# Kernel tuning notes

Measured on AMD Instinct MI355X. Metric: run time of the kernel, lower is better.

## Reference

```python
import jax, jax.numpy as jnp
import numpy as np

NUM_ITER = 8  # num_iterations


def kernel_to_freq_2d(kernel, H, W):
    """Place a (C, kh, kw) kernel circularly centered at origin on an (H, W) grid, then FFT."""
    C, kh, kw = kernel.shape
    th = (jnp.arange(kh) - kh // 2) % H
    tw = (jnp.arange(kw) - kw // 2) % W
    TH, TW = jnp.meshgrid(th, tw, indexing='ij')
    padded = jnp.zeros((C, H, W), dtype=kernel.dtype).at[:, TH, TW].set(kernel)
    return jnp.fft.fft2(padded, axes=(1, 2))  # (C, H, W) complex


def setup_inputs() -> dict:
    key = jax.random.key(0)
    k1, k2, k3 = jax.random.split(key, 3)
    B, H, W, C, k = 8, 256, 256, 64, 7
    x = jax.random.normal(k1, (B, H, W, C), dtype=jnp.float32)
    # gate_kernel is zeros-init in the module; use small random values so the
    # gate path is non-degenerate while keeping identical math.
    gate_kernel = jax.random.normal(k2, (C, k, k), dtype=jnp.float32) * 0.02
    # hidden_kernel: lecun_normal over fan_in = k*k (param shape (C, k, k))
    hidden_kernel = jax.random.normal(k3, (C, k, k), dtype=jnp.float32) * (1.0 / np.sqrt(k * k))
    return {"x": x, "gate_kernel": gate_kernel, "hidden_kernel": hidden_kernel}


def reference(x, gate_kernel, hidden_kernel):
    B, H, W, C = x.shape
    # Frequency-domain depthwise kernels, laid out (H, W, C) to match channels-last state.
    gate_f = kernel_to_freq_2d(gate_kernel, H, W).transpose(1, 2, 0)
    hidden_f = kernel_to_freq_2d(hidden_kernel, H, W).transpose(1, 2, 0)

    def step(h, _):
        # FFT over spatial dims (equivalent to the original's transpose->fft->transpose).
        h_f = jnp.fft.fft2(h, axes=(1, 2))  # (B, H, W, C) complex
        z = jax.nn.sigmoid(jnp.fft.ifft2(gate_f[None] * h_f, axes=(1, 2)).real)
        h_tilde = jnp.fft.ifft2(hidden_f[None] * h_f, axes=(1, 2)).real
        h_new = (1 - z) * h + z * h_tilde
        return h_new, None

    h_final, _ = jax.lax.scan(step, x, None, length=NUM_ITER)
    return h_final.astype(x.dtype)
```

## Files before the change

### kernel.cpp

```cpp
#include <hip/hip_runtime.h>


#define HH 256
#define WW 256
#define CC 64
#define TH 8
#define BC 128
#define LHT (TH + 6)
#define LWT (BC + 6)
#define PLANE (LHT * LWT)
#define WOFF (4 * PLANE)
#define LDS_FLOATS (WOFF + 196)

__global__ __launch_bounds__(256, 4) void gated_step(
    const float* __restrict__ src,
    const float* __restrict__ wg_g,
    const float* __restrict__ wh_g,
    float* __restrict__ dst)
{
    __shared__ float lds[LDS_FLOATS];

    const int tid = threadIdx.x;
    const int x   = tid & 63;
    const int w   = __builtin_amdgcn_readfirstlane(tid >> 6);

    const int id  = (int)blockIdx.x;
    const int nid = ((id & 7) << 10) | (id >> 3);
    const int cg  = nid & 15;
    const int xs  = (nid >> 4) & 1;
    const int ys  = (nid >> 5) & 31;
    const int b   = nid >> 10;
    const int x0  = xs * BC;
    const int y0  = ys * TH;
    const int ch  = (cg << 2) | w;

    float sw[49];
    #pragma unroll
    for (int t = 0; t < 49; ++t)
        sw[t] = __int_as_float(
            __builtin_amdgcn_readfirstlane(__float_as_int(wg_g[ch * 49 + t])));

    const float4* __restrict__ src4 = reinterpret_cast<const float4*>(src);
    for (int k = tid; k < PLANE; k += 256) {
        int col = k % LWT;
        int row = k / LWT;
        int gy = (y0 + row - 3) & 255;
        int gx = (x0 + col - 3) & 255;
        float4 v4 = src4[((((b << 8) + gy) << 8) + gx) * 16 + cg];
        lds[0 * PLANE + k] = v4.x;
        lds[1 * PLANE + k] = v4.y;
        lds[2 * PLANE + k] = v4.z;
        lds[3 * PLANE + k] = v4.w;
    }
    if (tid < 196) lds[WOFF + tid] = wh_g[cg * 196 + tid];
    __syncthreads();

    float wh[49];
    #pragma unroll
    for (int t = 0; t < 49; ++t) wh[t] = lds[WOFF + w * 49 + t];

    const float* plane = &lds[w * PLANE];
    float accg[2][TH], acch[2][TH];
    #pragma unroll
    for (int r = 0; r < TH; ++r) {
        accg[0][r] = 0.0f; accg[1][r] = 0.0f;
        acch[0][r] = 0.0f; acch[1][r] = 0.0f;
    }

    #pragma unroll
    for (int iy = 0; iy < LHT; ++iy) {
        float v[8];
        const float* rowp = plane + iy * LWT + 2 * x;
        #pragma unroll
        for (int m = 0; m < 4; ++m) {
            float2 t2 = *reinterpret_cast<const float2*>(rowp + 2 * m);
            v[2 * m]     = t2.x;
            v[2 * m + 1] = t2.y;
        }
        #pragma unroll
        for (int r = 0; r < TH; ++r) {
            const int i = r + 6 - iy;
            if (i >= 0 && i <= 6) {
                #pragma unroll
                for (int jv = 0; jv < 7; ++jv) {
                    const float a = sw[i * 7 + (6 - jv)];
                    const float h = wh[i * 7 + (6 - jv)];
                    accg[0][r] = fmaf(a, v[jv],     accg[0][r]);
                    acch[0][r] = fmaf(h, v[jv],     acch[0][r]);
                    accg[1][r] = fmaf(a, v[jv + 1], accg[1][r]);
                    acch[1][r] = fmaf(h, v[jv + 1], acch[1][r]);
                }
            }
        }
    }

    float hn[2][TH];
    #pragma unroll
    for (int r = 0; r < TH; ++r) {
        float c0 = plane[(r + 3) * LWT + 2 * x + 3];
        float c1 = plane[(r + 3) * LWT + 2 * x + 4];
        float e0 = __expf(-accg[0][r]);
        float e1 = __expf(-accg[1][r]);
        float z0 = __builtin_amdgcn_rcpf(1.0f + e0);
        float z1 = __builtin_amdgcn_rcpf(1.0f + e1);
        hn[0][r] = fmaf(z0, acch[0][r] - c0, c0);
        hn[1][r] = fmaf(z1, acch[1][r] - c1, c1);
    }
    __syncthreads();

    #pragma unroll
    for (int r = 0; r < TH; ++r) {
        float2 p; p.x = hn[0][r]; p.y = hn[1][r];
        *reinterpret_cast<float2*>(&lds[w * 1024 + r * 128 + 2 * x]) = p;
    }
    __syncthreads();

    float4* __restrict__ dst4 = reinterpret_cast<float4*>(dst);
    #pragma unroll
    for (int k2 = 0; k2 < 4; ++k2) {
        int pos = tid + k2 * 256;
        int c2  = pos & 127;
        int r   = pos >> 7;
        float4 o;
        o.x = lds[0 * 1024 + r * 128 + c2];
        o.y = lds[1 * 1024 + r * 128 + c2];
        o.z = lds[2 * 1024 + r * 128 + c2];
        o.w = lds[3 * 1024 + r * 128 + c2];
        dst4[((((b << 8) + (y0 + r)) << 8) + (x0 + c2)) * 16 + cg] = o;
    }
}

extern "C" void kernel_launch(void* const* d_in, const int* in_sizes, int n_in,
                              void* d_out, int out_size, void* d_ws, size_t ws_size,
                              hipStream_t stream) {
    const float* x  = (const float*)d_in[0];
    const float* wg = (const float*)d_in[1];
    const float* wh = (const float*)d_in[2];
    float* out = (float*)d_out;
    float* ws  = (float*)d_ws;

    dim3 grid(8 * 32 * 2 * 16);
    dim3 block(256);

    const float* src = x;
    for (int it = 0; it < 8; ++it) {
        float* dst = (it & 1) ? out : ws;
        gated_step<<<grid, block, 0, stream>>>(src, wg, wh, dst);
        src = dst;
    }
}
```

Before: 1.167 ms.

## Split gate and hidden convolutions across separate wave groups per block

Doubles the block to 512 threads so that four waves compute the gate convolution and four compute the hidden convolution, each holding only one 49-tap weight set and one accumulator set. Gate waves write sigmoid values to LDS, and hidden waves read them and combine with the center values cached during the row loop. The aim is to cut per-thread register pressure and raise occupancy and parallelism. The cost is an extra LDS round-trip and extra barriers, and the input tile is now loaded once for eight waves that do the same total FMA work.

```diff
diff --git a/kernel.cpp b/kernel.cpp
--- a/kernel.cpp
+++ b/kernel.cpp
@@ -9,10 +9,11 @@
 #define LHT (TH + 6)
 #define LWT (BC + 6)
 #define PLANE (LHT * LWT)
-#define WOFF (4 * PLANE)
-#define LDS_FLOATS (WOFF + 196)
+#define ZOFF 0
+#define HOFF 4096
+#define LDS_FLOATS 8192
 
-__global__ __launch_bounds__(256, 4) void gated_step(
+__global__ __launch_bounds__(512, 8) void gated_step(
     const float* __restrict__ src,
     const float* __restrict__ wg_g,
     const float* __restrict__ wh_g,
@@ -20,9 +21,11 @@
 {
     __shared__ float lds[LDS_FLOATS];
 
-    const int tid = threadIdx.x;
-    const int x   = tid & 63;
-    const int w   = __builtin_amdgcn_readfirstlane(tid >> 6);
+    const int tid  = threadIdx.x;
+    const int x    = tid & 63;
+    const int w    = __builtin_amdgcn_readfirstlane(tid >> 6);
+    const int cw   = w & 3;
+    const int role = w >> 2;
 
     const int id  = (int)blockIdx.x;
     const int nid = ((id & 7) << 10) | (id >> 3);
@@ -32,16 +35,10 @@
     const int b   = nid >> 10;
     const int x0  = xs * BC;
     const int y0  = ys * TH;
-    const int ch  = (cg << 2) | w;
-
-    float sw[49];
-    #pragma unroll
-    for (int t = 0; t < 49; ++t)
-        sw[t] = __int_as_float(
-            __builtin_amdgcn_readfirstlane(__float_as_int(wg_g[ch * 49 + t])));
+    const int ch  = (cg << 2) | cw;
 
     const float4* __restrict__ src4 = reinterpret_cast<const float4*>(src);
-    for (int k = tid; k < PLANE; k += 256) {
+    for (int k = tid; k < PLANE; k += 512) {
         int col = k % LWT;
         int row = k / LWT;
         int gy = (y0 + row - 3) & 255;
@@ -52,20 +49,21 @@
         lds[2 * PLANE + k] = v4.z;
         lds[3 * PLANE + k] = v4.w;
     }
-    if (tid < 196) lds[WOFF + tid] = wh_g[cg * 196 + tid];
+
+    const float* __restrict__ tbl = role ? wh_g : wg_g;
+    float sw[49];
+    #pragma unroll
+    for (int t = 0; t < 49; ++t)
+        sw[t] = __int_as_float(
+            __builtin_amdgcn_readfirstlane(__float_as_int(tbl[ch * 49 + t])));
+
     __syncthreads();
 
-    float wh[49];
+    const float* plane = &lds[cw * PLANE];
+    float acc[2][TH];
     #pragma unroll
-    for (int t = 0; t < 49; ++t) wh[t] = lds[WOFF + w * 49 + t];
-
-    const float* plane = &lds[w * PLANE];
-    float accg[2][TH], acch[2][TH];
-    #pragma unroll
-    for (int r = 0; r < TH; ++r) {
-        accg[0][r] = 0.0f; accg[1][r] = 0.0f;
-        acch[0][r] = 0.0f; acch[1][r] = 0.0f;
-    }
+    for (int r = 0; r < TH; ++r) { acc[0][r] = 0.0f; acc[1][r] = 0.0f; }
+    float ctr0[TH], ctr1[TH];
 
     #pragma unroll
     for (int iy = 0; iy < LHT; ++iy) {
@@ -77,6 +75,10 @@
             v[2 * m]     = t2.x;
             v[2 * m + 1] = t2.y;
         }
+        if (role && iy >= 3 && iy < 3 + TH) {
+            ctr0[iy - 3] = v[3];
+            ctr1[iy - 3] = v[4];
+        }
         #pragma unroll
         for (int r = 0; r < TH; ++r) {
             const int i = r + 6 - iy;
@@ -84,48 +86,52 @@
                 #pragma unroll
                 for (int jv = 0; jv < 7; ++jv) {
                     const float a = sw[i * 7 + (6 - jv)];
-                    const float h = wh[i * 7 + (6 - jv)];
-                    accg[0][r] = fmaf(a, v[jv],     accg[0][r]);
-                    acch[0][r] = fmaf(h, v[jv],     acch[0][r]);
-                    accg[1][r] = fmaf(a, v[jv + 1], accg[1][r]);
-                    acch[1][r] = fmaf(h, v[jv + 1], acch[1][r]);
+                    acc[0][r] = fmaf(a, v[jv],     acc[0][r]);
+                    acc[1][r] = fmaf(a, v[jv + 1], acc[1][r]);
                 }
             }
         }
     }
 
-    float hn[2][TH];
-    #pragma unroll
-    for (int r = 0; r < TH; ++r) {
-        float c0 = plane[(r + 3) * LWT + 2 * x + 3];
-        float c1 = plane[(r + 3) * LWT + 2 * x + 4];
-        float e0 = __expf(-accg[0][r]);
-        float e1 = __expf(-accg[1][r]);
-        float z0 = __builtin_amdgcn_rcpf(1.0f + e0);
-        float z1 = __builtin_amdgcn_rcpf(1.0f + e1);
-        hn[0][r] = fmaf(z0, acch[0][r] - c0, c0);
-        hn[1][r] = fmaf(z1, acch[1][r] - c1, c1);
+    __syncthreads();
+
+    if (role == 0) {
+        #pragma unroll
+        for (int r = 0; r < TH; ++r) {
+            float e0 = __expf(-acc[0][r]);
+            float e1 = __expf(-acc[1][r]);
+            float2 z;
+            z.x = __builtin_amdgcn_rcpf(1.0f + e0);
+            z.y = __builtin_amdgcn_rcpf(1.0f + e1);
+            *reinterpret_cast<float2*>(&lds[ZOFF + cw * 1024 + r * 128 + 2 * x]) = z;
+        }
     }
     __syncthreads();
 
-    #pragma unroll
-    for (int r = 0; r < TH; ++r) {
-        float2 p; p.x = hn[0][r]; p.y = hn[1][r];
-        *reinterpret_cast<float2*>(&lds[w * 1024 + r * 128 + 2 * x]) = p;
+    if (role == 1) {
+        #pragma unroll
+        for (int r = 0; r < TH; ++r) {
+            float2 z = *reinterpret_cast<const float2*>(
+                &lds[ZOFF + cw * 1024 + r * 128 + 2 * x]);
+            float2 hn;
+            hn.x = fmaf(z.x, acc[0][r] - ctr0[r], ctr0[r]);
+            hn.y = fmaf(z.y, acc[1][r] - ctr1[r], ctr1[r]);
+            *reinterpret_cast<float2*>(&lds[HOFF + cw * 1024 + r * 128 + 2 * x]) = hn;
+        }
     }
     __syncthreads();
 
     float4* __restrict__ dst4 = reinterpret_cast<float4*>(dst);
     #pragma unroll
-    for (int k2 = 0; k2 < 4; ++k2) {
-        int pos = tid + k2 * 256;
+    for (int k2 = 0; k2 < 2; ++k2) {
+        int pos = tid + k2 * 512;
         int c2  = pos & 127;
         int r   = pos >> 7;
         float4 o;
-        o.x = lds[0 * 1024 + r * 128 + c2];
-        o.y = lds[1 * 1024 + r * 128 + c2];
-        o.z = lds[2 * 1024 + r * 128 + c2];
-        o.w = lds[3 * 1024 + r * 128 + c2];
+        o.x = lds[HOFF + 0 * 1024 + r * 128 + c2];
+        o.y = lds[HOFF + 1 * 1024 + r * 128 + c2];
+        o.z = lds[HOFF + 2 * 1024 + r * 128 + c2];
+        o.w = lds[HOFF + 3 * 1024 + r * 128 + c2];
         dst4[((((b << 8) + (y0 + r)) << 8) + (x0 + c2)) * 16 + cg] = o;
     }
 }
@@ -140,7 +146,7 @@
     float* ws  = (float*)d_ws;
 
     dim3 grid(8 * 32 * 2 * 16);
-    dim3 block(256);
+    dim3 block(512);
 
     const float* src = x;
     for (int it = 0; it < 8; ++it) {
```

Result: slower. 1.997 ms (+71.1%).
